# Kernel optimization log

Measured on AMD Instinct MI355X. Metric: run time of the kernel, lower is better.

Reference implementation:

```python
import jax, jax.numpy as jnp
import numpy as np

EPS = 1e-8


def setup_inputs() -> dict:
    key = jax.random.key(0)
    k1, k2, k3 = jax.random.split(key, 3)
    K_, M, N = 2048, 512, 64
    x = jax.random.normal(k1, (K_, M), dtype=jnp.float32)
    w_att = jax.random.uniform(k2, (M, M), dtype=jnp.float32)
    w_b = jax.random.uniform(k3, (M, N), dtype=jnp.float32)
    return {"x": x, "w_att": w_att, "w_b": w_b, "l": 8}


def reference(x, w_att, w_b, l):
    # soft attention scores over features: [k, m]
    scores_soft = jax.nn.softmax(x @ w_att, axis=-1) + EPS
    # per-target l-th largest value of w_b over the m axis -> threshold [n]
    thr = jax.lax.top_k(w_b.T, l)[0][:, -1]  # [n]
    sh = w_b - thr[None, :] + EPS  # [m, n]
    # training-phase soft hard-mask: clamp to [-1, 1], shift to [0, 1]
    scores_hard = (jnp.clip(sh, -1.0, 1.0) + 1.0) * 0.5  # [m, n]
    # outer-product combine: 'mn,km->kmn' then 'kmn,km->kmn'
    mask_weight = scores_hard[None, :, :] * scores_soft[:, :, None]  # [k, m, n]
    out = mask_weight * x[:, :, None]  # [k, m, n]
    return out, scores_hard, scores_soft, mask_weight
```

## Files before the change

kernel.cpp:

```cpp
#include <hip/hip_runtime.h>
#include <math.h>

#define K_DIM 2048
#define M_DIM 512
#define N_DIM 64
#define EPSF 1e-8f

typedef float f32x4 __attribute__((ext_vector_type(4)));

__global__ __launch_bounds__(256) void thr_hard_kernel(
    const float* __restrict__ w_b, const int* __restrict__ lptr,
    float* __restrict__ scores_hard) {
  __shared__ float col[M_DIM];
  __shared__ float red[256];
  const int n = blockIdx.x;
  const int t = threadIdx.x;
  const int L = lptr[0];

  col[t]       = w_b[t * N_DIM + n];
  col[t + 256] = w_b[(t + 256) * N_DIM + n];
  __syncthreads();

  const float v0 = col[t], v1 = col[t + 256];
  int c0 = 0, c1 = 0;
  for (int i = 0; i < M_DIM; ++i) {
    const float c = col[i];
    c0 += (c > v0);
    c1 += (c > v1);
  }
  float cand0 = (c0 <= L - 1) ? v0 : INFINITY;
  float cand1 = (c1 <= L - 1) ? v1 : INFINITY;
  red[t] = fminf(cand0, cand1);
  __syncthreads();
  for (int s = 128; s > 0; s >>= 1) {
    if (t < s) red[t] = fminf(red[t], red[t + s]);
    __syncthreads();
  }
  const float thr = red[0];

  {
    float sh0 = (col[t] - thr) + EPSF;
    float sh1 = (col[t + 256] - thr) + EPSF;
    sh0 = fminf(fmaxf(sh0, -1.0f), 1.0f);
    sh1 = fminf(fmaxf(sh1, -1.0f), 1.0f);
    scores_hard[t * N_DIM + n]         = (sh0 + 1.0f) * 0.5f;
    scores_hard[(t + 256) * N_DIM + n] = (sh1 + 1.0f) * 0.5f;
  }
}

__global__ __launch_bounds__(256) void gemm_kernel(
    const float* __restrict__ x, const float* __restrict__ w,
    float* __restrict__ S) {
  __shared__ float xs[8][M_DIM];
  const int t = threadIdx.x;
  const int k0 = blockIdx.x * 8;

#pragma unroll
  for (int i = 0; i < 16; ++i) {
    const int idx = i * 256 + t;
    const int r = idx >> 9, c = idx & (M_DIM - 1);
    xs[r][c] = x[(k0 + r) * M_DIM + c];
  }
  __syncthreads();

  float acc0[8], acc1[8];
#pragma unroll
  for (int r = 0; r < 8; ++r) { acc0[r] = 0.0f; acc1[r] = 0.0f; }

  const int j0 = t, j1 = t + 256;
  for (int m = 0; m < M_DIM; m += 4) {
    const float w00 = w[(m + 0) * M_DIM + j0];
    const float w01 = w[(m + 1) * M_DIM + j0];
    const float w02 = w[(m + 2) * M_DIM + j0];
    const float w03 = w[(m + 3) * M_DIM + j0];
    const float w10 = w[(m + 0) * M_DIM + j1];
    const float w11 = w[(m + 1) * M_DIM + j1];
    const float w12 = w[(m + 2) * M_DIM + j1];
    const float w13 = w[(m + 3) * M_DIM + j1];
#pragma unroll
    for (int r = 0; r < 8; ++r) {
      const float4 xv = *(const float4*)&xs[r][m];
      acc0[r] += xv.x * w00 + xv.y * w01 + xv.z * w02 + xv.w * w03;
      acc1[r] += xv.x * w10 + xv.y * w11 + xv.z * w12 + xv.w * w13;
    }
  }

#pragma unroll
  for (int r = 0; r < 8; ++r) {
    S[(k0 + r) * M_DIM + j0] = acc0[r];
    S[(k0 + r) * M_DIM + j1] = acc1[r];
  }
}

__global__ __launch_bounds__(256) void softmax_kernel(float* __restrict__ S) {
  __shared__ float red[256];
  const int row = blockIdx.x, t = threadIdx.x;
  const float s0 = S[row * M_DIM + t];
  const float s1 = S[row * M_DIM + t + 256];

  red[t] = fmaxf(s0, s1);
  __syncthreads();
  for (int s = 128; s > 0; s >>= 1) {
    if (t < s) red[t] = fmaxf(red[t], red[t + s]);
    __syncthreads();
  }
  const float mx = red[0];
  __syncthreads();

  const float e0 = expf(s0 - mx);
  const float e1 = expf(s1 - mx);
  red[t] = e0 + e1;
  __syncthreads();
  for (int s = 128; s > 0; s >>= 1) {
    if (t < s) red[t] += red[t + s];
    __syncthreads();
  }
  const float inv = 1.0f / red[0];
  S[row * M_DIM + t]       = e0 * inv + EPSF;
  S[row * M_DIM + t + 256] = e1 * inv + EPSF;
}

__global__ __launch_bounds__(256) void combine_kernel(
    const float* __restrict__ x, const float* __restrict__ hard,
    const float* __restrict__ soft, f32x4* __restrict__ out,
    f32x4* __restrict__ mw) {
  const int gid = blockIdx.x * 256 + threadIdx.x;
  const int pair = gid >> 4;
  const int q = gid & 15;
  const int m = pair & (M_DIM - 1);

  const float ss = soft[pair];
  const float xv = x[pair];
  const f32x4 sh = *(const f32x4*)&hard[m * N_DIM + q * 4];

  f32x4 w = sh * ss;
  f32x4 o = w * xv;

  __builtin_nontemporal_store(o, &out[gid]);
  __builtin_nontemporal_store(w, &mw[gid]);
}

extern "C" void kernel_launch(void* const* d_in, const int* in_sizes, int n_in,
                              void* d_out, int out_size, void* d_ws,
                              size_t ws_size, hipStream_t stream) {
  const float* x     = (const float*)d_in[0];
  const float* w_att = (const float*)d_in[1];
  const float* w_b   = (const float*)d_in[2];
  const int*   lptr  = (const int*)d_in[3];

  float* out_base = (float*)d_out;
  const size_t OUT_SZ = (size_t)K_DIM * M_DIM * N_DIM;
  float* out0 = out_base;
  float* hard = out0 + OUT_SZ;
  float* soft = hard + (size_t)M_DIM * N_DIM;
  float* mwp  = soft + (size_t)K_DIM * M_DIM;

  thr_hard_kernel<<<N_DIM, 256, 0, stream>>>(w_b, lptr, hard);
  gemm_kernel<<<K_DIM / 8, 256, 0, stream>>>(x, w_att, soft);
  softmax_kernel<<<K_DIM, 256, 0, stream>>>(soft);

  const int total4 = K_DIM * M_DIM * 16;
  combine_kernel<<<total4 / 256, 256, 0, stream>>>(
      x, hard, soft, (f32x4*)out0, (f32x4*)mwp);
}
```

Measured before the change: 609.3 us.

## Fuse GEMM, softmax and outer-product combine into one kernel

```diff
diff --git a/kernel.cpp b/kernel.cpp
--- a/kernel.cpp
+++ b/kernel.cpp
@@ -5,6 +5,8 @@
 #define M_DIM 512
 #define N_DIM 64
 #define EPSF 1e-8f
+#define ROWS 8
+#define TPB 512
 
 typedef float f32x4 __attribute__((ext_vector_type(4)));
 
@@ -48,96 +50,92 @@
   }
 }
 
-__global__ __launch_bounds__(256) void gemm_kernel(
+__global__ __launch_bounds__(TPB) void fused_kernel(
     const float* __restrict__ x, const float* __restrict__ w,
-    float* __restrict__ S) {
-  __shared__ float xs[8][M_DIM];
+    const float* __restrict__ hard, float* __restrict__ soft,
+    f32x4* __restrict__ out, f32x4* __restrict__ mw) {
+  __shared__ float xs[ROWS][M_DIM];
+  __shared__ float sm[ROWS][M_DIM];
   const int t = threadIdx.x;
-  const int k0 = blockIdx.x * 8;
+  const int k0 = blockIdx.x * ROWS;
 
-#pragma unroll
-  for (int i = 0; i < 16; ++i) {
-    const int idx = i * 256 + t;
-    const int r = idx >> 9, c = idx & (M_DIM - 1);
-    xs[r][c] = x[(k0 + r) * M_DIM + c];
+  {
+    const f32x4* xg = (const f32x4*)(x + (size_t)k0 * M_DIM);
+    f32x4* xsv = (f32x4*)&xs[0][0];
+    xsv[t]       = xg[t];
+    xsv[t + TPB] = xg[t + TPB];
   }
   __syncthreads();
 
-  float acc0[8], acc1[8];
+  float acc[ROWS];
 #pragma unroll
-  for (int r = 0; r < 8; ++r) { acc0[r] = 0.0f; acc1[r] = 0.0f; }
+  for (int r = 0; r < ROWS; ++r) acc[r] = 0.0f;
 
-  const int j0 = t, j1 = t + 256;
+#pragma unroll 2
   for (int m = 0; m < M_DIM; m += 4) {
-    const float w00 = w[(m + 0) * M_DIM + j0];
-    const float w01 = w[(m + 1) * M_DIM + j0];
-    const float w02 = w[(m + 2) * M_DIM + j0];
-    const float w03 = w[(m + 3) * M_DIM + j0];
-    const float w10 = w[(m + 0) * M_DIM + j1];
-    const float w11 = w[(m + 1) * M_DIM + j1];
-    const float w12 = w[(m + 2) * M_DIM + j1];
-    const float w13 = w[(m + 3) * M_DIM + j1];
+    const float w0 = w[(m + 0) * M_DIM + t];
+    const float w1 = w[(m + 1) * M_DIM + t];
+    const float w2 = w[(m + 2) * M_DIM + t];
+    const float w3 = w[(m + 3) * M_DIM + t];
 #pragma unroll
-    for (int r = 0; r < 8; ++r) {
+    for (int r = 0; r < ROWS; ++r) {
       const float4 xv = *(const float4*)&xs[r][m];
-      acc0[r] += xv.x * w00 + xv.y * w01 + xv.z * w02 + xv.w * w03;
-      acc1[r] += xv.x * w10 + xv.y * w11 + xv.z * w12 + xv.w * w13;
+      acc[r] += xv.x * w0 + xv.y * w1 + xv.z * w2 + xv.w * w3;
     }
   }
-
 #pragma unroll
-  for (int r = 0; r < 8; ++r) {
-    S[(k0 + r) * M_DIM + j0] = acc0[r];
-    S[(k0 + r) * M_DIM + j1] = acc1[r];
-  }
-}
-
-__global__ __launch_bounds__(256) void softmax_kernel(float* __restrict__ S) {
-  __shared__ float red[256];
-  const int row = blockIdx.x, t = threadIdx.x;
-  const float s0 = S[row * M_DIM + t];
-  const float s1 = S[row * M_DIM + t + 256];
-
-  red[t] = fmaxf(s0, s1);
-  __syncthreads();
-  for (int s = 128; s > 0; s >>= 1) {
-    if (t < s) red[t] = fmaxf(red[t], red[t + s]);
-    __syncthreads();
-  }
-  const float mx = red[0];
+  for (int r = 0; r < ROWS; ++r) sm[r][t] = acc[r];
   __syncthreads();
 
-  const float e0 = expf(s0 - mx);
-  const float e1 = expf(s1 - mx);
-  red[t] = e0 + e1;
+  {
+    const int r = t >> 6, ln = t & 63;
+    float v[8];
+    float mx = -INFINITY;
+#pragma unroll
+    for (int i = 0; i < 8; ++i) {
+      v[i] = sm[r][ln + 64 * i];
+      mx = fmaxf(mx, v[i]);
+    }
+#pragma unroll
+    for (int s = 32; s > 0; s >>= 1) mx = fmaxf(mx, __shfl_xor(mx, s));
+    float sum = 0.0f;
+#pragma unroll
+    for (int i = 0; i < 8; ++i) {
+      v[i] = expf(v[i] - mx);
+      sum += v[i];
+    }
+#pragma unroll
+    for (int s = 32; s > 0; s >>= 1) sum += __shfl_xor(sum, s);
+    const float inv = 1.0f / sum;
+#pragma unroll
+    for (int i = 0; i < 8; ++i) sm[r][ln + 64 * i] = v[i] * inv + EPSF;
+  }
   __syncthreads();
-  for (int s = 128; s > 0; s >>= 1) {
-    if (t < s) red[t] += red[t + s];
-    __syncthreads();
+
+  {
+    const f32x4* smv = (const f32x4*)&sm[0][0];
+    f32x4* sg = (f32x4*)(soft + (size_t)k0 * M_DIM);
+    __builtin_nontemporal_store(smv[t], &sg[t]);
+    __builtin_nontemporal_store(smv[t + TPB], &sg[t + TPB]);
   }
-  const float inv = 1.0f / red[0];
-  S[row * M_DIM + t]       = e0 * inv + EPSF;
-  S[row * M_DIM + t + 256] = e1 * inv + EPSF;
-}
 
-__global__ __launch_bounds__(256) void combine_kernel(
-    const float* __restrict__ x, const float* __restrict__ hard,
-    const float* __restrict__ soft, f32x4* __restrict__ out,
-    f32x4* __restrict__ mw) {
-  const int gid = blockIdx.x * 256 + threadIdx.x;
-  const int pair = gid >> 4;
-  const int q = gid & 15;
-  const int m = pair & (M_DIM - 1);
-
-  const float ss = soft[pair];
-  const float xv = x[pair];
-  const f32x4 sh = *(const f32x4*)&hard[m * N_DIM + q * 4];
-
-  f32x4 w = sh * ss;
-  f32x4 o = w * xv;
-
-  __builtin_nontemporal_store(o, &out[gid]);
-  __builtin_nontemporal_store(w, &mw[gid]);
+  const f32x4* hard4 = (const f32x4*)hard;
+  const size_t base = (size_t)k0 * (M_DIM * (N_DIM / 4));
+#pragma unroll 4
+  for (int it = 0; it < (ROWS * M_DIM * 16) / TPB; ++it) {
+    const int g = it * TPB + t;
+    const int q = g & 15;
+    const int pair = g >> 4;
+    const int m = pair & (M_DIM - 1);
+    const int r = pair >> 9;
+    const float ss = sm[r][m];
+    const float xv = xs[r][m];
+    const f32x4 sh = hard4[m * 16 + q];
+    const f32x4 wgt = sh * ss;
+    const f32x4 o = wgt * xv;
+    __builtin_nontemporal_store(o, &out[base + g]);
+    __builtin_nontemporal_store(wgt, &mw[base + g]);
+  }
 }
 
 extern "C" void kernel_launch(void* const* d_in, const int* in_sizes, int n_in,
@@ -156,10 +154,6 @@
   float* mwp  = soft + (size_t)K_DIM * M_DIM;
 
   thr_hard_kernel<<<N_DIM, 256, 0, stream>>>(w_b, lptr, hard);
-  gemm_kernel<<<K_DIM / 8, 256, 0, stream>>>(x, w_att, soft);
-  softmax_kernel<<<K_DIM, 256, 0, stream>>>(soft);
-
-  const int total4 = K_DIM * M_DIM * 16;
-  combine_kernel<<<total4 / 256, 256, 0, stream>>>(
-      x, hard, soft, (f32x4*)out0, (f32x4*)mwp);
+  fused_kernel<<<K_DIM / ROWS, TPB, 0, stream>>>(
+      x, w_att, hard, soft, (f32x4*)out0, (f32x4*)mwp);
 }
```

Measured after the change: 615.6 us. No clear change (+1.0%).
